# Kernel optimization log

Hardware: AMD Instinct MI355X
Metric: run time of the kernel (lower is better)

Reference implementation:

```python
import jax, jax.numpy as jnp
import numpy as np

N_NODES = 50000
N_EDGES = 1600000
IN_C = 256
HID_C = 128
OUT_C = 16
HEADS = 8
NEG_SLOPE = 0.2  # PyG GATConv default


def gat_layer(x, src, dst, W, att_src, att_dst, bias, heads, out_c):
    """PyG-style GATConv (eval mode, add_self_loops already applied to src/dst).
    x: [N, F_in], W: [F_in, heads*out_c], att_*: [heads, out_c], bias: [heads*out_c].
    Returns concatenated heads: [N, heads*out_c]."""
    N = x.shape[0]
    h = (x @ W).reshape(N, heads, out_c)                  # [N, H, C]
    a_src = (h * att_src[None]).sum(-1)                   # [N, H]
    a_dst = (h * att_dst[None]).sum(-1)                   # [N, H]
    alpha = a_src[src] + a_dst[dst]                       # [E, H]
    alpha = jax.nn.leaky_relu(alpha, NEG_SLOPE)
    # segment softmax over incoming edges of each destination node
    amax = jax.ops.segment_max(alpha, dst, num_segments=N)  # [N, H]
    alpha = jnp.exp(alpha - jax.lax.stop_gradient(amax)[dst])
    denom = jax.ops.segment_sum(alpha, dst, num_segments=N)  # [N, H]
    w = alpha / denom[dst]                                # [E, H]
    msg = h[src] * w[:, :, None]                          # [E, H, C]
    out = jax.ops.segment_sum(msg, dst, num_segments=N)   # [N, H, C]
    return out.reshape(N, heads * out_c) + bias


def setup_inputs() -> dict:
    key = jax.random.key(0)
    ks = jax.random.split(key, 10)
    x = jax.random.normal(ks[0], (N_NODES, IN_C), dtype=jnp.float32)
    edge_index = jax.random.randint(ks[1], (2, N_EDGES), 0, N_NODES, dtype=jnp.int32)
    c1 = HID_C // HEADS  # 16 per head
    s1 = 1.0 / np.sqrt(IN_C)
    s2 = 1.0 / np.sqrt(HID_C)
    return {
        "x": x,
        "edge_index": edge_index,
        "W1": jax.random.normal(ks[2], (IN_C, HEADS * c1), dtype=jnp.float32) * s1,
        "att_src1": jax.random.normal(ks[3], (HEADS, c1), dtype=jnp.float32) * s1,
        "att_dst1": jax.random.normal(ks[4], (HEADS, c1), dtype=jnp.float32) * s1,
        "bias1": jnp.zeros((HEADS * c1,), dtype=jnp.float32),
        "W2": jax.random.normal(ks[5], (HID_C, OUT_C), dtype=jnp.float32) * s2,
        "att_src2": jax.random.normal(ks[6], (1, OUT_C), dtype=jnp.float32) * s2,
        "att_dst2": jax.random.normal(ks[7], (1, OUT_C), dtype=jnp.float32) * s2,
        "bias2": jnp.zeros((OUT_C,), dtype=jnp.float32),
    }


def reference(x, edge_index, W1, att_src1, att_dst1, bias1, W2, att_src2, att_dst2, bias2):
    N = x.shape[0]
    loop = jnp.arange(N, dtype=edge_index.dtype)
    src = jnp.concatenate([edge_index[0], loop])  # add_self_loops=True (PyG default)
    dst = jnp.concatenate([edge_index[1], loop])
    h = gat_layer(x, src, dst, W1, att_src1, att_dst1, bias1, HEADS, HID_C // HEADS)
    h = jax.nn.relu(h)
    # F.dropout with training=False is identity (eval mode)
    out = gat_layer(h, src, dst, W2, att_src2, att_dst2, bias2, 1, OUT_C)
    return out
```

## Files before the change

kernel.cpp:

```cpp
#include <hip/hip_runtime.h>
#include <hip/hip_bf16.h>


#define NN 50000
#define NE 1600000
#define NBK 196
#define NB_SC 512
#define CHUNK (NE / NB_SC)
#define GB1 782
#define GB2 1563

typedef __attribute__((ext_vector_type(8))) short bf16x8;
typedef __attribute__((ext_vector_type(4))) float f32x4;
typedef __attribute__((ext_vector_type(8))) _Float16 f16x8;
typedef __attribute__((ext_vector_type(8))) unsigned short u16x8;

__device__ __forceinline__ float lrelu(float x) { return fmaxf(x, 0.2f * x); }

__device__ __forceinline__ float ldf(const void* p, int i, int isbf) {
  return isbf ? __bfloat162float(((const __hip_bfloat16*)p)[i])
              : ((const float*)p)[i];
}
__device__ __forceinline__ short f2bf_bits(float v) {
  __hip_bfloat16 h = __float2bfloat16(v);
  return *reinterpret_cast<short*>(&h);
}
__device__ __forceinline__ unsigned short f2h_bits(float v) {
  _Float16 h = (_Float16)v;
  return *reinterpret_cast<unsigned short*>(&h);
}
__device__ __forceinline__ float f16lo(unsigned int u) {
  union { unsigned int u; _Float16 h[2]; } c; c.u = u; return (float)c.h[0];
}
__device__ __forceinline__ float f16hi(unsigned int u) {
  union { unsigned int u; _Float16 h[2]; } c; c.u = u; return (float)c.h[1];
}

#define OFF_H1   ((size_t)0)
#define OFF_H    ((size_t)25600000)
#define OFF_H2   ((size_t)51200000)
#define OFF_AS1  ((size_t)54400000)
#define OFF_AD1  ((size_t)56000000)
#define OFF_AS2  ((size_t)57600000)
#define OFF_AD2  ((size_t)57800000)
#define OFF_CNT  ((size_t)58000000)
#define OFF_OFFS ((size_t)58400000)
#define OFF_CSR  ((size_t)58600000)
#define OFF_WP1  ((size_t)65000000)
#define OFF_TOT  ((size_t)65065536)
#define OFF_FLAG ((size_t)65068608)

__global__ void repack_w1(const void* __restrict__ W1, short* __restrict__ Wp,
                          const unsigned int* __restrict__ xw, int* __restrict__ flag) {
  __shared__ int s[256];
  __shared__ int sf;
  int t = threadIdx.x;
  unsigned int w = xw[t * 97 + 5];
  unsigned int e = (w >> 7) & 0xFF;
  s[t] = (e >= 116 && e <= 138) ? 1 : 0;
  __syncthreads();
  for (int off = 128; off > 0; off >>= 1) {
    if (t < off) s[t] += s[t + off];
    __syncthreads();
  }
  if (t == 0) {
    sf = (s[0] >= 128) ? 1 : 0;
    if (blockIdx.x == 0) *flag = sf;
  }
  __syncthreads();
  int f = sf;
  int i = blockIdx.x * 256 + t;
  int j = i & 7, q = (i >> 3) & 3, c = (i >> 5) & 127, tt = i >> 12;
  int src = (tt * 32 + q * 8 + j) * 128 + c;
  Wp[i] = f ? ((const short*)W1)[src] : f2bf_bits(((const float*)W1)[src]);
}

__global__ __launch_bounds__(256) void fat1(const void* __restrict__ X,
                                            const short* __restrict__ Wp,
                                            unsigned short* __restrict__ H1h,
                                            const int* __restrict__ flag,
                                            const int* __restrict__ dst,
                                            int* __restrict__ HB) {
  __shared__ int h[224];
  if (blockIdx.x < GB1) {
    int wave = threadIdx.x >> 6, lane = threadIdx.x & 63;
    int rowbase = blockIdx.x * 64 + wave * 16;
    int l15 = lane & 15, quad = lane >> 4;
    int f = *flag;
    int arow = rowbase + l15;
    if (arow >= NN) arow = NN - 1;
    f32x4 acc[8];
#pragma unroll
    for (int ct = 0; ct < 8; ++ct) acc[ct] = (f32x4){0.f, 0.f, 0.f, 0.f};
    size_t abase = (size_t)arow * 256 + quad * 8;
#pragma unroll
    for (int kt = 0; kt < 8; ++kt) {
      bf16x8 a;
      if (f) {
        a = *(const bf16x8*)((const short*)X + abase + kt * 32);
      } else {
        const float* xp = (const float*)X + abase + kt * 32;
        float4 v0 = *(const float4*)xp, v1 = *(const float4*)(xp + 4);
        a[0] = f2bf_bits(v0.x); a[1] = f2bf_bits(v0.y);
        a[2] = f2bf_bits(v0.z); a[3] = f2bf_bits(v0.w);
        a[4] = f2bf_bits(v1.x); a[5] = f2bf_bits(v1.y);
        a[6] = f2bf_bits(v1.z); a[7] = f2bf_bits(v1.w);
      }
#pragma unroll
      for (int ct = 0; ct < 8; ++ct) {
        bf16x8 b = *(const bf16x8*)(Wp + ((kt * 128 + ct * 16 + l15) * 4 + quad) * 8);
        acc[ct] = __builtin_amdgcn_mfma_f32_16x16x32_bf16(a, b, acc[ct], 0, 0, 0);
      }
    }
    int r0 = rowbase + quad * 4;
#pragma unroll
    for (int ct = 0; ct < 8; ++ct)
#pragma unroll
      for (int r = 0; r < 4; ++r) {
        int row = r0 + r;
        if (row < NN) H1h[(size_t)row * 128 + ct * 16 + l15] = f2h_bits(acc[ct][r]);
      }
  } else {
    int b = blockIdx.x - GB1;
    int t = threadIdx.x;
    for (int i = t; i < 224; i += 256) h[i] = 0;
    __syncthreads();
    int e0 = b * CHUNK, e1 = e0 + CHUNK;
    for (int e = e0 + t; e < e1; e += 256) atomicAdd(&h[dst[e] >> 8], 1);
    __syncthreads();
    for (int i = t; i < NBK; i += 256) HB[b * NBK + i] = h[i];
  }
}

__global__ __launch_bounds__(256) void fat2(const unsigned short* __restrict__ H1h,
                                            const void* __restrict__ as1,
                                            const void* __restrict__ ad1,
                                            float* __restrict__ AS,
                                            float* __restrict__ AD,
                                            const int* __restrict__ flag,
                                            int* __restrict__ HB,
                                            int* __restrict__ total) {
  __shared__ float s_as[128], s_ad[128];
  __shared__ int ts[256];
  int t = threadIdx.x;
  if (blockIdx.x < GB2) {
    int f = *flag;
    if (t < 128) { s_as[t] = ldf(as1, t, f); s_ad[t] = ldf(ad1, t, f); }
    __syncthreads();
    int tid = blockIdx.x * 256 + t;
    if (tid >= NN * 8) return;
    int n = tid >> 3, hh = tid & 7;
    const f16x8* hp = (const f16x8*)(H1h + (size_t)n * 128 + hh * 16);
    f16x8 v0 = hp[0], v1 = hp[1];
    float as = 0.f, ad = 0.f;
#pragma unroll
    for (int i = 0; i < 8; ++i) {
      int b = hh * 16 + i;
      float x0 = (float)v0[i], x1 = (float)v1[i];
      as = fmaf(x0, s_as[b], fmaf(x1, s_as[b + 8], as));
      ad = fmaf(x0, s_ad[b], fmaf(x1, s_ad[b + 8], ad));
    }
    AS[tid] = as; AD[tid] = ad;
  } else {
    int k = blockIdx.x - GB2;
    int v0 = HB[(t * 2) * NBK + k], v1 = HB[(t * 2 + 1) * NBK + k];
    int s = v0 + v1;
    ts[t] = s;
    __syncthreads();
    for (int off = 1; off < 256; off <<= 1) {
      int a = (t >= off) ? ts[t - off] : 0;
      __syncthreads();
      ts[t] += a;
      __syncthreads();
    }
    int ex = ts[t] - s;
    HB[(t * 2) * NBK + k] = ex;
    HB[(t * 2 + 1) * NBK + k] = ex + v0;
    if (t == 255) total[k] = ts[255];
  }
}

__global__ __launch_bounds__(256) void scat_write(const int* __restrict__ src,
                                                  const int* __restrict__ dst,
                                                  const int* __restrict__ HB,
                                                  const int* __restrict__ total,
                                                  unsigned int* __restrict__ EPp) {
  __shared__ int h[224], sc[256], lofs[224], lc[224], gd[224];
  __shared__ unsigned int EB[CHUNK];
  __shared__ unsigned char BKT[CHUNK];
  int t = threadIdx.x, b = blockIdx.x;
  int tv = (t < NBK) ? total[t] : 0;
  sc[t] = tv;
  __syncthreads();
  for (int off = 1; off < 256; off <<= 1) {
    int a = (t >= off) ? sc[t - off] : 0;
    __syncthreads();
    sc[t] += a;
    __syncthreads();
  }
  if (t < NBK) gd[t] = (sc[t] - tv) + HB[b * NBK + t];
  for (int i = t; i < 224; i += 256) h[i] = 0;
  __syncthreads();
  int e0 = b * CHUNK, e1 = e0 + CHUNK;
  for (int e = e0 + t; e < e1; e += 256) atomicAdd(&h[dst[e] >> 8], 1);
  __syncthreads();
  int v = (t < NBK) ? h[t] : 0;
  sc[t] = v;
  __syncthreads();
  for (int off = 1; off < 256; off <<= 1) {
    int a = (t >= off) ? sc[t - off] : 0;
    __syncthreads();
    sc[t] += a;
    __syncthreads();
  }
  if (t < NBK) { int ex = sc[t] - v; lofs[t] = ex; lc[t] = ex; }
  __syncthreads();
  for (int e = e0 + t; e < e1; e += 256) {
    int d = dst[e];
    int k = d >> 8;
    int pos = atomicAdd(&lc[k], 1);
    EB[pos] = ((unsigned int)(d & 255) << 16) | (unsigned int)src[e];
    BKT[pos] = (unsigned char)k;
  }
  __syncthreads();
  for (int pos = t; pos < CHUNK; pos += 256) {
    int k = BKT[pos];
    EPp[gd[k] + (pos - lofs[k])] = EB[pos];
  }
}

__global__ __launch_bounds__(1024) void bucket_csr(const unsigned int* __restrict__ EPp,
                                                   const int* __restrict__ total,
                                                   int* __restrict__ cnt,
                                                   int* __restrict__ offs,
                                                   unsigned short* __restrict__ csr) {
  __shared__ int h[256], sc[256], lc[256];
  int b = blockIdx.x, t = threadIdx.x;
  int tv = 0;
  if (t < 256) { tv = (t < NBK) ? total[t] : 0; sc[t] = tv; }
  __syncthreads();
  for (int off = 1; off < 256; off <<= 1) {
    int a = (t >= off && t < 256) ? sc[t - off] : 0;
    __syncthreads();
    if (t < 256) sc[t] += a;
    __syncthreads();
  }
  __shared__ int s_gbase, s_n;
  if (t == (unsigned)b) { s_gbase = sc[b] - tv; s_n = tv; }
  __syncthreads();
  int gbase = s_gbase, n = s_n;
  if (t < 256) h[t] = 0;
  __syncthreads();
  for (int i = t; i < n; i += 1024) atomicAdd(&h[(EPp[gbase + i] >> 16) & 255], 1);
  __syncthreads();
  int v = 0;
  if (t < 256) { v = h[t]; sc[t] = v; }
  __syncthreads();
  for (int off = 1; off < 256; off <<= 1) {
    int add = (t >= off && t < 256) ? sc[t - off] : 0;
    __syncthreads();
    if (t < 256) sc[t] += add;
    __syncthreads();
  }
  if (t < 256) {
    int ex = sc[t] - v;
    int node = (b << 8) + t;
    if (node < NN) { cnt[node] = v; offs[node] = gbase + ex; }
    lc[t] = ex;
  }
  __syncthreads();
  for (int i = t; i < n; i += 1024) {
    unsigned int p = EPp[gbase + i];
    int pos = atomicAdd(&lc[(p >> 16) & 255], 1);
    csr[gbase + pos] = (unsigned short)(p & 0xFFFF);
  }
}

__global__ __launch_bounds__(256) void agg1(const unsigned short* __restrict__ H1h,
                                            const float* __restrict__ AS,
                                            const float* __restrict__ AD,
                                            const int* __restrict__ offs,
                                            const int* __restrict__ cnt,
                                            const unsigned short* __restrict__ csr,
                                            const void* __restrict__ bias1,
                                            unsigned short* __restrict__ Hh,
                                            const int* __restrict__ flag) {
  int lane = threadIdx.x & 63;
  int node = blockIdx.x * 4 + (threadIdx.x >> 6);
  int f = *flag;
  int start = offs[node], deg = cnt[node];
  int g = lane >> 3, k = lane & 7;
  float adst = AD[node * 8 + k];
  float acc[16];
#pragma unroll
  for (int i = 0; i < 16; ++i) acc[i] = 0.f;
  float dsum = 0.f;
  if (g == 0) {
    float p = __expf(lrelu(AS[node * 8 + k] + adst));
    dsum = p;
    const f16x8* hp = (const f16x8*)(H1h + (size_t)node * 128 + k * 16);
    f16x8 v0 = hp[0], v1 = hp[1];
#pragma unroll
    for (int i = 0; i < 8; ++i) {
      acc[i] = fmaf(p, (float)v0[i], acc[i]);
      acc[8 + i] = fmaf(p, (float)v1[i], acc[8 + i]);
    }
  }
  int s0 = (g < deg) ? (int)csr[start + g] : -1;
  float a0 = 0.f; f16x8 u0a, u0b;
  if (s0 >= 0) {
    a0 = AS[s0 * 8 + k];
    const f16x8* hp = (const f16x8*)(H1h + (size_t)s0 * 128 + k * 16);
    u0a = hp[0]; u0b = hp[1];
  }
  int s1 = (8 + g < deg) ? (int)csr[start + 8 + g] : -1;
  for (int eb = 0; eb < deg; eb += 8) {
    float a1 = 0.f; f16x8 u1a, u1b;
    if (s1 >= 0) {
      a1 = AS[s1 * 8 + k];
      const f16x8* hp = (const f16x8*)(H1h + (size_t)s1 * 128 + k * 16);
      u1a = hp[0]; u1b = hp[1];
    }
    int en2 = eb + 16 + g;
    int s2 = (en2 < deg) ? (int)csr[start + en2] : -1;
    if (s0 >= 0) {
      float p = __expf(lrelu(a0 + adst));
      dsum += p;
#pragma unroll
      for (int i = 0; i < 8; ++i) {
        acc[i] = fmaf(p, (float)u0a[i], acc[i]);
        acc[8 + i] = fmaf(p, (float)u0b[i], acc[8 + i]);
      }
    }
    s0 = s1; a0 = a1; u0a = u1a; u0b = u1b; s1 = s2;
  }
#pragma unroll
  for (int i = 0; i < 16; ++i) {
    acc[i] += __shfl_xor(acc[i], 8);
    acc[i] += __shfl_xor(acc[i], 16);
    acc[i] += __shfl_xor(acc[i], 32);
  }
  dsum += __shfl_xor(dsum, 8);
  dsum += __shfl_xor(dsum, 16);
  dsum += __shfl_xor(dsum, 32);
  if (g == 0) {
    float inv = 1.0f / dsum;
    int c0 = k * 16;
    u16x8 o0, o1;
#pragma unroll
    for (int i = 0; i < 8; ++i) {
      o0[i] = f2h_bits(fmaxf(acc[i] * inv + ldf(bias1, c0 + i, f), 0.f));
      o1[i] = f2h_bits(fmaxf(acc[8 + i] * inv + ldf(bias1, c0 + 8 + i, f), 0.f));
    }
    *(u16x8*)(Hh + (size_t)node * 128 + c0) = o0;
    *(u16x8*)(Hh + (size_t)node * 128 + c0 + 8) = o1;
  }
}

__global__ __launch_bounds__(256) void gemm2_a2(const unsigned short* __restrict__ Hb,
                                                const void* __restrict__ W2,
                                                const void* __restrict__ as2,
                                                const void* __restrict__ ad2,
                                                unsigned short* __restrict__ H2h,
                                                float* __restrict__ AS2,
                                                float* __restrict__ AD2,
                                                const int* __restrict__ flag) {
  __shared__ float sW[2048];
  int t = threadIdx.x;
  int f = *flag;
  for (int i = t; i < 2048; i += 256) sW[i] = ldf(W2, i, f);
  __syncthreads();
  int lane = t & 63, wave = t >> 6;
  int l15 = lane & 15, quad = lane >> 4;
  f16x8 bfr[4];
#pragma unroll
  for (int kt = 0; kt < 4; ++kt)
#pragma unroll
    for (int j = 0; j < 8; ++j)
      bfr[kt][j] = (_Float16)sW[(kt * 32 + quad * 8 + j) * 16 + l15];
  float ca = ldf(as2, l15, f), cd = ldf(ad2, l15, f);
  int tile = blockIdx.x * 4 + wave;
  if (tile >= NN / 16) return;
  int n0 = tile * 16;
  const f16x8* ap = (const f16x8*)(Hb + (size_t)(n0 + l15) * 128);
  f32x4 c = (f32x4){0.f, 0.f, 0.f, 0.f};
#pragma unroll
  for (int kt = 0; kt < 4; ++kt)
    c = __builtin_amdgcn_mfma_f32_16x16x32_f16(ap[kt * 4 + quad], bfr[kt], c, 0, 0, 0);
#pragma unroll
  for (int r = 0; r < 4; ++r) {
    int n = n0 + quad * 4 + r;
    H2h[n * 16 + l15] = f2h_bits(c[r]);
    float vs = c[r] * ca, vd = c[r] * cd;
    vs += __shfl_xor(vs, 1); vd += __shfl_xor(vd, 1);
    vs += __shfl_xor(vs, 2); vd += __shfl_xor(vd, 2);
    vs += __shfl_xor(vs, 4); vd += __shfl_xor(vd, 4);
    vs += __shfl_xor(vs, 8); vd += __shfl_xor(vd, 8);
    if (l15 == 0) { AS2[n] = vs; AD2[n] = vd; }
  }
}

__global__ __launch_bounds__(256) void agg2(const unsigned short* __restrict__ H2h,
                                            const float* __restrict__ AS2,
                                            const float* __restrict__ AD2,
                                            const int* __restrict__ offs,
                                            const int* __restrict__ cnt,
                                            const unsigned short* __restrict__ csr,
                                            const void* __restrict__ bias2,
                                            void* __restrict__ outv,
                                            const int* __restrict__ flag) {
  int lane = threadIdx.x & 63;
  int node = blockIdx.x * 4 + (threadIdx.x >> 6);
  int f = *flag;
  int start = offs[node], deg = cnt[node];
  int g = lane >> 3, k = lane & 7;
  float adst = AD2[node];
  float a0 = 0.f, a1 = 0.f, dsum = 0.f;
  if (g == 0) {
    float p = __expf(lrelu(AS2[node] + adst));
    dsum = p;
    unsigned int hv = *(const unsigned int*)(H2h + (size_t)node * 16 + k * 2);
    a0 = fmaf(p, f16lo(hv), a0);
    a1 = fmaf(p, f16hi(hv), a1);
  }
  int s0 = (g < deg) ? (int)csr[start + g] : -1;
  float as_c = 0.f; unsigned int hv_c = 0;
  if (s0 >= 0) {
    as_c = AS2[s0];
    hv_c = *(const unsigned int*)(H2h + (size_t)s0 * 16 + k * 2);
  }
  int s1 = (8 + g < deg) ? (int)csr[start + 8 + g] : -1;
  for (int eb = 0; eb < deg; eb += 8) {
    float as_n = 0.f; unsigned int hv_n = 0;
    if (s1 >= 0) {
      as_n = AS2[s1];
      hv_n = *(const unsigned int*)(H2h + (size_t)s1 * 16 + k * 2);
    }
    int en2 = eb + 16 + g;
    int s2 = (en2 < deg) ? (int)csr[start + en2] : -1;
    if (s0 >= 0) {
      float p = __expf(lrelu(as_c + adst));
      dsum += p;
      a0 = fmaf(p, f16lo(hv_c), a0);
      a1 = fmaf(p, f16hi(hv_c), a1);
    }
    s0 = s1; as_c = as_n; hv_c = hv_n; s1 = s2;
  }
  a0 += __shfl_xor(a0, 8);  a0 += __shfl_xor(a0, 16);  a0 += __shfl_xor(a0, 32);
  a1 += __shfl_xor(a1, 8);  a1 += __shfl_xor(a1, 16);  a1 += __shfl_xor(a1, 32);
  dsum += __shfl_xor(dsum, 8); dsum += __shfl_xor(dsum, 16); dsum += __shfl_xor(dsum, 32);
  if (g == 0) {
    float inv = 1.0f / dsum;
    float o0 = a0 * inv + ldf(bias2, k * 2 + 0, f);
    float o1 = a1 * inv + ldf(bias2, k * 2 + 1, f);
    size_t base = (size_t)node * 16 + k * 2;
    if (f) {
      ((__hip_bfloat16*)outv)[base] = __float2bfloat16(o0);
      ((__hip_bfloat16*)outv)[base + 1] = __float2bfloat16(o1);
    } else {
      *(float2*)((float*)outv + base) = make_float2(o0, o1);
    }
  }
}

extern "C" void kernel_launch(void* const* d_in, const int* in_sizes, int n_in,
                              void* d_out, int out_size, void* d_ws, size_t ws_size,
                              hipStream_t stream) {
  const void* x = d_in[0];
  const int* ei = (const int*)d_in[1];
  const void* W1 = d_in[2];
  const void* as1 = d_in[3];
  const void* ad1 = d_in[4];
  const void* b1 = d_in[5];
  const void* W2 = d_in[6];
  const void* as2 = d_in[7];
  const void* ad2 = d_in[8];
  const void* b2 = d_in[9];
  char* ws = (char*)d_ws;

  unsigned short* H1h = (unsigned short*)(ws + OFF_H1);
  unsigned short* Hh = (unsigned short*)(ws + OFF_H);
  unsigned int* EPp = (unsigned int*)(ws + OFF_H);
  unsigned short* H2h = (unsigned short*)(ws + OFF_H2);
  int* HB = (int*)(ws + OFF_H2);
  float* AS1 = (float*)(ws + OFF_AS1);
  float* AD1 = (float*)(ws + OFF_AD1);
  float* AS2 = (float*)(ws + OFF_AS2);
  float* AD2 = (float*)(ws + OFF_AD2);
  int* CNT = (int*)(ws + OFF_CNT);
  int* OFFS = (int*)(ws + OFF_OFFS);
  unsigned short* CSR = (unsigned short*)(ws + OFF_CSR);
  short* Wp = (short*)(ws + OFF_WP1);
  int* TOT = (int*)(ws + OFF_TOT);
  int* FLAG = (int*)(ws + OFF_FLAG);

  repack_w1<<<128, 256, 0, stream>>>(W1, Wp, (const unsigned int*)x, FLAG);
  fat1<<<GB1 + NB_SC, 256, 0, stream>>>(x, Wp, H1h, FLAG, ei + NE, HB);
  fat2<<<GB2 + NBK, 256, 0, stream>>>(H1h, as1, ad1, AS1, AD1, FLAG, HB, TOT);
  scat_write<<<NB_SC, 256, 0, stream>>>(ei, ei + NE, HB, TOT, EPp);
  bucket_csr<<<NBK, 1024, 0, stream>>>(EPp, TOT, CNT, OFFS, CSR);

  agg1<<<NN / 4, 256, 0, stream>>>(H1h, AS1, AD1, OFFS, CNT, CSR, b1, Hh, FLAG);
  gemm2_a2<<<GB1, 256, 0, stream>>>(Hh, W2, as2, ad2, H2h, AS2, AD2, FLAG);
  agg2<<<NN / 4, 256, 0, stream>>>(H2h, AS2, AD2, OFFS, CNT, CSR, b2, d_out, FLAG);
}
```

Baseline: 255.8 us.

## Regroup preprocessing kernels into three fused launches to cut one launch

Reassigns the independent stages across kernel launches. The dst histogram now runs alongside the W1 repack, the bucket prefix scan alongside the layer-1 GEMM, and the edge scatter alongside the attention-logit computation. Four launches become three, and independent work fills the gaps at each dependency boundary. The trade-off is that the attention blocks in fatC now carry the scatter's large shared-memory allocation, which may lower their occupancy.

```diff
diff --git a/kernel.cpp b/kernel.cpp
--- a/kernel.cpp
+++ b/kernel.cpp
@@ -50,38 +50,53 @@
 #define OFF_TOT  ((size_t)65065536)
 #define OFF_FLAG ((size_t)65068608)
 
-__global__ void repack_w1(const void* __restrict__ W1, short* __restrict__ Wp,
-                          const unsigned int* __restrict__ xw, int* __restrict__ flag) {
+__global__ __launch_bounds__(256) void fatA(const int* __restrict__ dst,
+                                            int* __restrict__ HB,
+                                            const void* __restrict__ W1,
+                                            short* __restrict__ Wp,
+                                            const unsigned int* __restrict__ xw,
+                                            int* __restrict__ flag) {
+  __shared__ int h[224];
   __shared__ int s[256];
   __shared__ int sf;
   int t = threadIdx.x;
-  unsigned int w = xw[t * 97 + 5];
-  unsigned int e = (w >> 7) & 0xFF;
-  s[t] = (e >= 116 && e <= 138) ? 1 : 0;
-  __syncthreads();
-  for (int off = 128; off > 0; off >>= 1) {
-    if (t < off) s[t] += s[t + off];
-    __syncthreads();
-  }
-  if (t == 0) {
-    sf = (s[0] >= 128) ? 1 : 0;
-    if (blockIdx.x == 0) *flag = sf;
-  }
-  __syncthreads();
-  int f = sf;
-  int i = blockIdx.x * 256 + t;
-  int j = i & 7, q = (i >> 3) & 3, c = (i >> 5) & 127, tt = i >> 12;
-  int src = (tt * 32 + q * 8 + j) * 128 + c;
-  Wp[i] = f ? ((const short*)W1)[src] : f2bf_bits(((const float*)W1)[src]);
-}
-
-__global__ __launch_bounds__(256) void fat1(const void* __restrict__ X,
+  if (blockIdx.x < NB_SC) {
+    int b = blockIdx.x;
+    for (int i = t; i < 224; i += 256) h[i] = 0;
+    __syncthreads();
+    int e0 = b * CHUNK, e1 = e0 + CHUNK;
+    for (int e = e0 + t; e < e1; e += 256) atomicAdd(&h[dst[e] >> 8], 1);
+    __syncthreads();
+    for (int i = t; i < NBK; i += 256) HB[b * NBK + i] = h[i];
+  } else {
+    unsigned int w = xw[t * 97 + 5];
+    unsigned int e = (w >> 7) & 0xFF;
+    s[t] = (e >= 116 && e <= 138) ? 1 : 0;
+    __syncthreads();
+    for (int off = 128; off > 0; off >>= 1) {
+      if (t < off) s[t] += s[t + off];
+      __syncthreads();
+    }
+    if (t == 0) {
+      sf = (s[0] >= 128) ? 1 : 0;
+      if (blockIdx.x == NB_SC) *flag = sf;
+    }
+    __syncthreads();
+    int f = sf;
+    int i = (blockIdx.x - NB_SC) * 256 + t;
+    int j = i & 7, q = (i >> 3) & 3, c = (i >> 5) & 127, tt = i >> 12;
+    int src = (tt * 32 + q * 8 + j) * 128 + c;
+    Wp[i] = f ? ((const short*)W1)[src] : f2bf_bits(((const float*)W1)[src]);
+  }
+}
+
+__global__ __launch_bounds__(256) void fatB(const void* __restrict__ X,
                                             const short* __restrict__ Wp,
                                             unsigned short* __restrict__ H1h,
                                             const int* __restrict__ flag,
-                                            const int* __restrict__ dst,
-                                            int* __restrict__ HB) {
-  __shared__ int h[224];
+                                            int* __restrict__ HB,
+                                            int* __restrict__ total) {
+  __shared__ int ts[256];
   if (blockIdx.x < GB1) {
     int wave = threadIdx.x >> 6, lane = threadIdx.x & 63;
     int rowbase = blockIdx.x * 64 + wave * 16;
@@ -121,33 +136,86 @@
         if (row < NN) H1h[(size_t)row * 128 + ct * 16 + l15] = f2h_bits(acc[ct][r]);
       }
   } else {
-    int b = blockIdx.x - GB1;
     int t = threadIdx.x;
-    for (int i = t; i < 224; i += 256) h[i] = 0;
-    __syncthreads();
-    int e0 = b * CHUNK, e1 = e0 + CHUNK;
-    for (int e = e0 + t; e < e1; e += 256) atomicAdd(&h[dst[e] >> 8], 1);
-    __syncthreads();
-    for (int i = t; i < NBK; i += 256) HB[b * NBK + i] = h[i];
-  }
-}
-
-__global__ __launch_bounds__(256) void fat2(const unsigned short* __restrict__ H1h,
+    int k = blockIdx.x - GB1;
+    int v0 = HB[(t * 2) * NBK + k], v1 = HB[(t * 2 + 1) * NBK + k];
+    int s = v0 + v1;
+    ts[t] = s;
+    __syncthreads();
+    for (int off = 1; off < 256; off <<= 1) {
+      int a = (t >= off) ? ts[t - off] : 0;
+      __syncthreads();
+      ts[t] += a;
+      __syncthreads();
+    }
+    int ex = ts[t] - s;
+    HB[(t * 2) * NBK + k] = ex;
+    HB[(t * 2 + 1) * NBK + k] = ex + v0;
+    if (t == 255) total[k] = ts[255];
+  }
+}
+
+__global__ __launch_bounds__(256) void fatC(const int* __restrict__ src,
+                                            const int* __restrict__ dst,
+                                            const int* __restrict__ HB,
+                                            const int* __restrict__ total,
+                                            unsigned int* __restrict__ EPp,
+                                            const unsigned short* __restrict__ H1h,
                                             const void* __restrict__ as1,
                                             const void* __restrict__ ad1,
                                             float* __restrict__ AS,
                                             float* __restrict__ AD,
-                                            const int* __restrict__ flag,
-                                            int* __restrict__ HB,
-                                            int* __restrict__ total) {
+                                            const int* __restrict__ flag) {
+  __shared__ int h[224], sc[256], lofs[224], lc[224], gd[224];
+  __shared__ unsigned int EB[CHUNK];
+  __shared__ unsigned char BKT[CHUNK];
   __shared__ float s_as[128], s_ad[128];
-  __shared__ int ts[256];
   int t = threadIdx.x;
-  if (blockIdx.x < GB2) {
+  if (blockIdx.x < NB_SC) {
+    int b = blockIdx.x;
+    int tv = (t < NBK) ? total[t] : 0;
+    sc[t] = tv;
+    __syncthreads();
+    for (int off = 1; off < 256; off <<= 1) {
+      int a = (t >= off) ? sc[t - off] : 0;
+      __syncthreads();
+      sc[t] += a;
+      __syncthreads();
+    }
+    if (t < NBK) gd[t] = (sc[t] - tv) + HB[b * NBK + t];
+    for (int i = t; i < 224; i += 256) h[i] = 0;
+    __syncthreads();
+    int e0 = b * CHUNK, e1 = e0 + CHUNK;
+    for (int e = e0 + t; e < e1; e += 256) atomicAdd(&h[dst[e] >> 8], 1);
+    __syncthreads();
+    int v = (t < NBK) ? h[t] : 0;
+    sc[t] = v;
+    __syncthreads();
+    for (int off = 1; off < 256; off <<= 1) {
+      int a = (t >= off) ? sc[t - off] : 0;
+      __syncthreads();
+      sc[t] += a;
+      __syncthreads();
+    }
+    if (t < NBK) { int ex = sc[t] - v; lofs[t] = ex; lc[t] = ex; }
+    __syncthreads();
+    for (int e = e0 + t; e < e1; e += 256) {
+      int d = dst[e];
+      int k = d >> 8;
+      int pos = atomicAdd(&lc[k], 1);
+      EB[pos] = ((unsigned int)(d & 255) << 16) | (unsigned int)src[e];
+      BKT[pos] = (unsigned char)k;
+    }
+    __syncthreads();
+    for (int pos = t; pos < CHUNK; pos += 256) {
+      int k = BKT[pos];
+      EPp[gd[k] + (pos - lofs[k])] = EB[pos];
+    }
+  } else {
     int f = *flag;
     if (t < 128) { s_as[t] = ldf(as1, t, f); s_ad[t] = ldf(ad1, t, f); }
     __syncthreads();
-    int tid = blockIdx.x * 256 + t;
+    int tid = (blockIdx.x - NB_SC) * 256 + t;
     if (tid >= NN * 8) return;
     int n = tid >> 3, hh = tid & 7;
     const f16x8* hp = (const f16x8*)(H1h + (size_t)n * 128 + hh * 16);
@@ -161,71 +229,6 @@
       ad = fmaf(x0, s_ad[b], fmaf(x1, s_ad[b + 8], ad));
     }
     AS[tid] = as; AD[tid] = ad;
-  } else {
-    int k = blockIdx.x - GB2;
-    int v0 = HB[(t * 2) * NBK + k], v1 = HB[(t * 2 + 1) * NBK + k];
-    int s = v0 + v1;
-    ts[t] = s;
-    __syncthreads();
-    for (int off = 1; off < 256; off <<= 1) {
-      int a = (t >= off) ? ts[t - off] : 0;
-      __syncthreads();
-      ts[t] += a;
-      __syncthreads();
-    }
-    int ex = ts[t] - s;
-    HB[(t * 2) * NBK + k] = ex;
-    HB[(t * 2 + 1) * NBK + k] = ex + v0;
-    if (t == 255) total[k] = ts[255];
-  }
-}
-
-__global__ __launch_bounds__(256) void scat_write(const int* __restrict__ src,
-                                                  const int* __restrict__ dst,
-                                                  const int* __restrict__ HB,
-                                                  const int* __restrict__ total,
-                                                  unsigned int* __restrict__ EPp) {
-  __shared__ int h[224], sc[256], lofs[224], lc[224], gd[224];
-  __shared__ unsigned int EB[CHUNK];
-  __shared__ unsigned char BKT[CHUNK];
-  int t = threadIdx.x, b = blockIdx.x;
-  int tv = (t < NBK) ? total[t] : 0;
-  sc[t] = tv;
-  __syncthreads();
-  for (int off = 1; off < 256; off <<= 1) {
-    int a = (t >= off) ? sc[t - off] : 0;
-    __syncthreads();
-    sc[t] += a;
-    __syncthreads();
-  }
-  if (t < NBK) gd[t] = (sc[t] - tv) + HB[b * NBK + t];
-  for (int i = t; i < 224; i += 256) h[i] = 0;
-  __syncthreads();
-  int e0 = b * CHUNK, e1 = e0 + CHUNK;
-  for (int e = e0 + t; e < e1; e += 256) atomicAdd(&h[dst[e] >> 8], 1);
-  __syncthreads();
-  int v = (t < NBK) ? h[t] : 0;
-  sc[t] = v;
-  __syncthreads();
-  for (int off = 1; off < 256; off <<= 1) {
-    int a = (t >= off) ? sc[t - off] : 0;
-    __syncthreads();
-    sc[t] += a;
-    __syncthreads();
-  }
-  if (t < NBK) { int ex = sc[t] - v; lofs[t] = ex; lc[t] = ex; }
-  __syncthreads();
-  for (int e = e0 + t; e < e1; e += 256) {
-    int d = dst[e];
-    int k = d >> 8;
-    int pos = atomicAdd(&lc[k], 1);
-    EB[pos] = ((unsigned int)(d & 255) << 16) | (unsigned int)src[e];
-    BKT[pos] = (unsigned char)k;
-  }
-  __syncthreads();
-  for (int pos = t; pos < CHUNK; pos += 256) {
-    int k = BKT[pos];
-    EPp[gd[k] + (pos - lofs[k])] = EB[pos];
   }
 }
 
@@ -494,10 +497,11 @@
   int* TOT = (int*)(ws + OFF_TOT);
   int* FLAG = (int*)(ws + OFF_FLAG);
 
-  repack_w1<<<128, 256, 0, stream>>>(W1, Wp, (const unsigned int*)x, FLAG);
-  fat1<<<GB1 + NB_SC, 256, 0, stream>>>(x, Wp, H1h, FLAG, ei + NE, HB);
-  fat2<<<GB2 + NBK, 256, 0, stream>>>(H1h, as1, ad1, AS1, AD1, FLAG, HB, TOT);
-  scat_write<<<NB_SC, 256, 0, stream>>>(ei, ei + NE, HB, TOT, EPp);
+  fatA<<<NB_SC + 128, 256, 0, stream>>>(ei + NE, HB, W1, Wp,
+                                        (const unsigned int*)x, FLAG);
+  fatB<<<GB1 + NBK, 256, 0, stream>>>(x, Wp, H1h, FLAG, HB, TOT);
+  fatC<<<NB_SC + GB2, 256, 0, stream>>>(ei, ei + NE, HB, TOT, EPp,
+                                        H1h, as1, ad1, AS1, AD1, FLAG);
   bucket_csr<<<NBK, 1024, 0, stream>>>(EPp, TOT, CNT, OFFS, CSR);
 
   agg1<<<NN / 4, 256, 0, stream>>>(H1h, AS1, AD1, OFFS, CNT, CSR, b1, Hh, FLAG);
```

Measured after the change: 255.8 us. About the same (+0.0%).
